# Kernel optimization log

Hardware: AMD Instinct MI355X
Metric: run time of the kernel (lower is better)

Reference implementation:

```python
import jax, jax.numpy as jnp
import numpy as np

NUM_HEADS = 4
OUTPUT_DIM = 32
NUM_NODES = 50000
NUM_EDGES = 800000
INPUT_DIM = 128


def setup_inputs() -> dict:
    key = jax.random.key(0)
    k1, k2, k3, k4 = jax.random.split(key, 4)
    node_features = jax.random.uniform(k1, (NUM_NODES, INPUT_DIM), dtype=jnp.float32)
    edge_index = jax.random.randint(k2, (2, NUM_EDGES), 0, NUM_NODES, dtype=jnp.int64)
    # Linear weight (xavier-like scale), stored as [in, out] for x @ W
    W = jax.random.normal(k3, (INPUT_DIM, NUM_HEADS * OUTPUT_DIM), dtype=jnp.float32) * 0.1
    att = jax.random.normal(k4, (2 * OUTPUT_DIM, 1), dtype=jnp.float32) * 0.2
    return {"node_features": node_features, "edge_index": edge_index, "W": W, "att": att}


def reference(node_features, edge_index, W, att):
    num_nodes = node_features.shape[0]
    # Linear projection -> [N, H, D]  (dropout = identity in eval mode)
    proj = (node_features @ W).reshape(num_nodes, NUM_HEADS, OUTPUT_DIM)
    src = proj[edge_index[0]]   # [E, H, D]
    tgt = proj[edge_index[1]]   # [E, H, D]
    # concat([src,tgt]) @ att  ==  src @ att[:D] + tgt @ att[D:]
    a_src = att[:OUTPUT_DIM, 0]   # [D]
    a_tgt = att[OUTPUT_DIM:, 0]   # [D]
    scores = jax.nn.leaky_relu(
        jnp.einsum('ehd,d->eh', src, a_src) + jnp.einsum('ehd,d->eh', tgt, a_tgt),
        negative_slope=0.01,
    )  # [E, H]
    # Faithful to original: softmax over the HEADS axis (dim=-1 of [E, H])
    alpha = jax.nn.softmax(scores, axis=-1)  # [E, H]
    weighted = tgt * alpha[..., None]        # [E, H, D]
    # index_add_ on dim 0 with edge_index[0]
    out = jax.ops.segment_sum(weighted, edge_index[0], num_segments=num_nodes)  # [N, H, D]
    # concat_heads=False -> mean over heads
    return out.mean(axis=1)  # [N, D]
```

## Files before the change

kernel.cpp:

```cpp
#include <hip/hip_runtime.h>
#include <math.h>

#define N_NODES 50000
#define N_EDGES 800000
#define IN_DIM 128
#define N_HEADS 4
#define OUT_DIM 32
#define PROJ_DIM 128
#define WSTR 144

#define NBIN 196
#define BINCAP 5000
#define MAXDEG 64

#define PROJ_BLKS 391
#define PART_BLKS 391
#define TOTAL_BLKS (PROJ_BLKS + PART_BLKS)

typedef short bf16x8 __attribute__((ext_vector_type(8)));
typedef float f32x4  __attribute__((ext_vector_type(4)));
typedef _Float16 h2  __attribute__((ext_vector_type(2)));

__device__ __forceinline__ ushort f32_to_bf16(float f) {
    unsigned u = __float_as_uint(f);
    unsigned r = u + 0x7fffu + ((u >> 16) & 1u);
    return (ushort)(r >> 16);
}

__device__ __forceinline__ float bf16_to_f32(ushort v) {
    return __uint_as_float((unsigned)v << 16);
}

__device__ __forceinline__ bf16x8 cvt8(float4 a, float4 b) {
    bf16x8 r;
    r[0] = (short)f32_to_bf16(a.x); r[1] = (short)f32_to_bf16(a.y);
    r[2] = (short)f32_to_bf16(a.z); r[3] = (short)f32_to_bf16(a.w);
    r[4] = (short)f32_to_bf16(b.x); r[5] = (short)f32_to_bf16(b.y);
    r[6] = (short)f32_to_bf16(b.z); r[7] = (short)f32_to_bf16(b.w);
    return r;
}

__global__ __launch_bounds__(256) void combo_kernel(
    const float* __restrict__ X, const float* __restrict__ W,
    const float* __restrict__ att, const int* __restrict__ ei,
    ushort* __restrict__ projT, float* __restrict__ s_src, float* __restrict__ s_tgt,
    int* __restrict__ bin_cursor, unsigned* __restrict__ slab)
{
    __shared__ ushort Wt[128 * WSTR];

    const int tid = threadIdx.x;

    if (blockIdx.x >= PROJ_BLKS) {
        int* cnt   = (int*)Wt;
        int* gbase = cnt + 256;

        for (int t = tid; t < NBIN; t += 256) cnt[t] = 0;
        __syncthreads();

        const int ebase = (blockIdx.x - PROJ_BLKS) * 2048;
        unsigned srcv[8], tgtv[8];
        int rank[8];
#pragma unroll
        for (int i = 0; i < 8; ++i) {
            int e = ebase + i * 256 + tid;
            bool ok = e < N_EDGES;
            srcv[i] = ok ? (unsigned)ei[e] : 0u;
            tgtv[i] = ok ? (unsigned)ei[N_EDGES + e] : 0u;
            rank[i] = ok ? atomicAdd(&cnt[srcv[i] >> 8], 1) : -1;
        }
        __syncthreads();

        for (int t = tid; t < NBIN; t += 256)
            gbase[t] = atomicAdd(&bin_cursor[t], cnt[t]);
        __syncthreads();

#pragma unroll
        for (int i = 0; i < 8; ++i) {
            if (rank[i] >= 0) {
                int bin = srcv[i] >> 8;
                int p = gbase[bin] + rank[i];
                if (p < BINCAP)
                    slab[bin * BINCAP + p] = (tgtv[i] << 16) | (srcv[i] & 255u);
            }
        }
        return;
    }

    for (int idx = tid; idx < 64 * 128; idx += 256) {
        int kp = idx >> 7;
        int c  = idx & 127;
        float w0 = W[(2 * kp) * PROJ_DIM + c];
        float w1 = W[(2 * kp + 1) * PROJ_DIM + c];
        unsigned pr = (unsigned)f32_to_bf16(w0) | ((unsigned)f32_to_bf16(w1) << 16);
        *(unsigned*)&Wt[c * WSTR + 2 * kp] = pr;
    }
    __syncthreads();

    const int wv   = tid >> 6;
    const int lane = tid & 63;
    const int m = lane & 15;
    const int q = lane >> 4;
    const int rbase = blockIdx.x * 128;

    int arow0 = rbase + wv * 32 + m;
    int arow1 = arow0 + 16;
    arow0 = (arow0 < N_NODES) ? arow0 : N_NODES - 1;
    arow1 = (arow1 < N_NODES) ? arow1 : N_NODES - 1;
    const long long xb0 = (long long)arow0 * IN_DIM;
    const long long xb1 = (long long)arow1 * IN_DIM;

    f32x4 acc[2][8];
#pragma unroll
    for (int rt = 0; rt < 2; ++rt)
#pragma unroll
        for (int ct = 0; ct < 8; ++ct) acc[rt][ct] = (f32x4){0.f, 0.f, 0.f, 0.f};

#pragma unroll
    for (int ks = 0; ks < 4; ++ks) {
        const int k0 = ks * 32 + q * 8;
        float4 a0lo = *(const float4*)&X[xb0 + k0];
        float4 a0hi = *(const float4*)&X[xb0 + k0 + 4];
        float4 a1lo = *(const float4*)&X[xb1 + k0];
        float4 a1hi = *(const float4*)&X[xb1 + k0 + 4];
        bf16x8 afrag0 = cvt8(a0lo, a0hi);
        bf16x8 afrag1 = cvt8(a1lo, a1hi);
#pragma unroll
        for (int ct = 0; ct < 8; ++ct) {
            bf16x8 bfrag = *(const bf16x8*)&Wt[(ct * 16 + m) * WSTR + k0];
            acc[0][ct] = __builtin_amdgcn_mfma_f32_16x16x32_bf16(afrag0, bfrag, acc[0][ct], 0, 0, 0);
            acc[1][ct] = __builtin_amdgcn_mfma_f32_16x16x32_bf16(afrag1, bfrag, acc[1][ct], 0, 0, 0);
        }
    }

    const float as_lo = att[m],      as_hi = att[m + 16];
    const float at_lo = att[32 + m], at_hi = att[48 + m];

#pragma unroll
    for (int rt = 0; rt < 2; ++rt) {
        const int rowb = rbase + wv * 32 + rt * 16 + q * 4;
#pragma unroll
        for (int r = 0; r < 4; ++r) {
            const int row = rowb + r;
            float cl[4], ch[4];
#pragma unroll
            for (int h = 0; h < 4; ++h) {
                cl[h] = acc[rt][2 * h][r];
                ch[h] = acc[rt][2 * h + 1][r];
            }
            if (row < N_NODES) {
                ushort4 plo, phi;
                plo.x = f32_to_bf16(cl[0]); plo.y = f32_to_bf16(cl[1]);
                plo.z = f32_to_bf16(cl[2]); plo.w = f32_to_bf16(cl[3]);
                phi.x = f32_to_bf16(ch[0]); phi.y = f32_to_bf16(ch[1]);
                phi.z = f32_to_bf16(ch[2]); phi.w = f32_to_bf16(ch[3]);
                *(ushort4*)&projT[(long long)row * PROJ_DIM + m * 4] = plo;
                *(ushort4*)&projT[(long long)row * PROJ_DIM + (m + 16) * 4] = phi;
            }
            float ps[4], pt[4];
#pragma unroll
            for (int h = 0; h < 4; ++h) {
                ps[h] = cl[h] * as_lo + ch[h] * as_hi;
                pt[h] = cl[h] * at_lo + ch[h] * at_hi;
            }
#pragma unroll
            for (int off = 8; off > 0; off >>= 1) {
#pragma unroll
                for (int h = 0; h < 4; ++h) {
                    ps[h] += __shfl_down(ps[h], off, 16);
                    pt[h] += __shfl_down(pt[h], off, 16);
                }
            }
            if (m == 0 && row < N_NODES) {
                *(float4*)&s_src[row * N_HEADS] = make_float4(ps[0], ps[1], ps[2], ps[3]);
                *(float4*)&s_tgt[row * N_HEADS] = make_float4(pt[0], pt[1], pt[2], pt[3]);
            }
        }
    }
}

__global__ __launch_bounds__(256) void binsort_kernel(
    const unsigned* __restrict__ slab, const int* __restrict__ bin_cursor,
    ushort* __restrict__ csr, int* __restrict__ offs, int* __restrict__ deg)
{
    __shared__ int cnt2[256];
    __shared__ int ex[256];
    __shared__ int wsum[4];
    __shared__ ushort stgt[BINCAP];

    const int b = blockIdx.x;
    const int t = threadIdx.x;
    const int lane = t & 63;
    const int wid  = t >> 6;
    int n_e = bin_cursor[b];
    n_e = (n_e < BINCAP) ? n_e : BINCAP;

    cnt2[t] = 0;
    __syncthreads();

    unsigned pk[20];
    int npk = 0;
    for (int i = t; i < n_e; i += 256) {
        unsigned v = slab[b * BINCAP + i];
        int node8 = v & 255u;
        int r = atomicAdd(&cnt2[node8], 1);
        r = (r < 255) ? r : 255;
        pk[npk++] = (v & 0xFFFF0000u) | ((unsigned)r << 8) | (unsigned)node8;
    }
    __syncthreads();

    const int v = cnt2[t];
    int x = v;
#pragma unroll
    for (int off = 1; off < 64; off <<= 1) {
        int y = __shfl_up(x, off);
        x += (lane >= off) ? y : 0;
    }
    if (lane == 63) wsum[wid] = x;
    __syncthreads();
    int add = 0;
#pragma unroll
    for (int w = 0; w < 4; ++w) add += (w < wid) ? wsum[w] : 0;
    ex[t] = x + add - v;
    __syncthreads();

    for (int j = 0; j < npk; ++j) {
        unsigned pv = pk[j];
        int lpos = ex[pv & 255u] + (int)((pv >> 8) & 255u);
        if (lpos < BINCAP) stgt[lpos] = (ushort)(pv >> 16);
    }
    __syncthreads();

    for (int i = t; i < n_e; i += 256) csr[b * BINCAP + i] = stgt[i];
    int node = b * 256 + t;
    if (node < N_NODES) {
        offs[node] = b * BINCAP + ex[t];
        deg[node]  = cnt2[t];
    }
}

__global__ __launch_bounds__(256) void gather_kernel(
    const int* __restrict__ deg, const int* __restrict__ offs,
    const ushort* __restrict__ csr,
    const float* __restrict__ s_src, const float* __restrict__ s_tgt,
    const ushort* __restrict__ projT, float* __restrict__ out)
{
    const int wv   = threadIdx.x >> 6;
    const int lane = threadIdx.x & 63;
    const int node = blockIdx.x * 4 + wv;

    int n = deg[node];
    n = (n < MAXDEG) ? n : MAXDEG;
    const int o = offs[node];

    int mytgt = 0, myA01 = 0, myA23 = 0;
    if (lane < n) {
        int tgt = csr[o + lane];
        float4 ss = *(const float4*)&s_src[node * N_HEADS];
        float4 st = *(const float4*)&s_tgt[tgt * N_HEADS];

        float sc[4] = { ss.x + st.x, ss.y + st.y, ss.z + st.z, ss.w + st.w };
        float mx = -1e30f;
#pragma unroll
        for (int h = 0; h < 4; ++h) {
            sc[h] = (sc[h] > 0.0f) ? sc[h] : 0.01f * sc[h];
            mx = fmaxf(mx, sc[h]);
        }
        float sum = 0.0f;
#pragma unroll
        for (int h = 0; h < 4; ++h) {
            sc[h] = __expf(sc[h] - mx);
            sum += sc[h];
        }
        float inv = 0.25f / sum;

        h2 a01, a23;
        a01.x = (_Float16)(sc[0] * inv);
        a01.y = (_Float16)(sc[1] * inv);
        a23.x = (_Float16)(sc[2] * inv);
        a23.y = (_Float16)(sc[3] * inv);
        mytgt = tgt;
        myA01 = __builtin_bit_cast(int, a01);
        myA23 = __builtin_bit_cast(int, a23);
    }

    const int d    = lane & 31;
    const int half = lane >> 5;

    float acc0 = 0.0f, acc1 = 0.0f, acc2 = 0.0f, acc3 = 0.0f;

    for (int j = 0; j < n; j += 16) {
        int tg[8], ea[8], eb[8];
#pragma unroll
        for (int u = 0; u < 8; ++u) {
            int sl = j + 2 * u + half;
            bool ok = sl < n;
            int slc = ok ? sl : 0;
            int tgv = __shfl(mytgt, slc);
            int eav = __shfl(myA01, slc);
            int ebv = __shfl(myA23, slc);
            tg[u] = tgv;
            ea[u] = ok ? eav : 0;
            eb[u] = ok ? ebv : 0;
        }
        ushort4 p[8];
#pragma unroll
        for (int u = 0; u < 8; ++u)
            p[u] = *(const ushort4*)&projT[(long long)tg[u] * PROJ_DIM + d * 4];
#pragma unroll
        for (int u = 0; u < 8; ++u) {
            h2 a = __builtin_bit_cast(h2, ea[u]);
            h2 b = __builtin_bit_cast(h2, eb[u]);
            float* accp = (u & 1) ? ((u & 2) ? &acc3 : &acc1)
                                  : ((u & 2) ? &acc2 : &acc0);
            float tt = *accp;
            tt = fmaf((float)a.x, bf16_to_f32(p[u].x), tt);
            tt = fmaf((float)a.y, bf16_to_f32(p[u].y), tt);
            tt = fmaf((float)b.x, bf16_to_f32(p[u].z), tt);
            tt = fmaf((float)b.y, bf16_to_f32(p[u].w), tt);
            *accp = tt;
        }
    }

    float acc = (acc0 + acc1) + (acc2 + acc3);
    acc += __shfl_down(acc, 32);
    if (lane < 32) out[node * OUT_DIM + d] = acc;
}

extern "C" void kernel_launch(void* const* d_in, const int* in_sizes, int n_in,
                              void* d_out, int out_size, void* d_ws, size_t ws_size,
                              hipStream_t stream) {
    const float* X   = (const float*)d_in[0];
    const int*   ei  = (const int*)d_in[1];
    const float* W   = (const float*)d_in[2];
    const float* att = (const float*)d_in[3];
    float* out = (float*)d_out;

    char* p = (char*)d_ws;
    ushort* projT   = (ushort*)p;   p += (size_t)N_NODES * PROJ_DIM * 2;
    float* s_src    = (float*)p;    p += (size_t)N_NODES * N_HEADS * 4;
    float* s_tgt    = (float*)p;    p += (size_t)N_NODES * N_HEADS * 4;
    unsigned* slab  = (unsigned*)p; p += (size_t)NBIN * BINCAP * 4;
    ushort* csr     = (ushort*)p;   p += (size_t)NBIN * BINCAP * 2;
    int* offs       = (int*)p;      p += (size_t)N_NODES * 4;
    int* deg        = (int*)p;      p += (size_t)N_NODES * 4;
    int* bin_cursor = (int*)p;      p += 256 * 4;

    (void)hipMemsetAsync(bin_cursor, 0, 256 * sizeof(int), stream);

    combo_kernel<<<TOTAL_BLKS, 256, 0, stream>>>(
        X, W, att, ei, projT, s_src, s_tgt, bin_cursor, slab);

    binsort_kernel<<<NBIN, 256, 0, stream>>>(slab, bin_cursor, csr, offs, deg);

    gather_kernel<<<N_NODES / 4, 256, 0, stream>>>(
        deg, offs, csr, s_src, s_tgt, projT, out);
}
```

Baseline: 145.2 us.

## Replace two-pass bin sort with direct per-node fixed-slot adjacency via global atomics

Drops the shared-memory binning pass and the separate binsort kernel. Each edge now claims a slot in a fixed 64-entry per-node adjacency array through a global atomicAdd on the node's degree counter. The gather kernel indexes that array by node*MAXDEG instead of a computed offset. This saves one kernel launch and the slab round trip, but adds about 800k global atomics with scattered 2-byte writes and a larger memset of the degree array.

```diff
diff --git a/kernel.cpp b/kernel.cpp
--- a/kernel.cpp
+++ b/kernel.cpp
@@ -9,8 +9,6 @@
 #define PROJ_DIM 128
 #define WSTR 144
 
-#define NBIN 196
-#define BINCAP 5000
 #define MAXDEG 64
 
 #define PROJ_BLKS 391
@@ -44,43 +42,23 @@
     const float* __restrict__ X, const float* __restrict__ W,
     const float* __restrict__ att, const int* __restrict__ ei,
     ushort* __restrict__ projT, float* __restrict__ s_src, float* __restrict__ s_tgt,
-    int* __restrict__ bin_cursor, unsigned* __restrict__ slab)
+    int* __restrict__ deg, ushort* __restrict__ csr)
 {
     __shared__ ushort Wt[128 * WSTR];
 
     const int tid = threadIdx.x;
 
     if (blockIdx.x >= PROJ_BLKS) {
-        int* cnt   = (int*)Wt;
-        int* gbase = cnt + 256;
-
-        for (int t = tid; t < NBIN; t += 256) cnt[t] = 0;
-        __syncthreads();
-
         const int ebase = (blockIdx.x - PROJ_BLKS) * 2048;
-        unsigned srcv[8], tgtv[8];
-        int rank[8];
 #pragma unroll
         for (int i = 0; i < 8; ++i) {
             int e = ebase + i * 256 + tid;
-            bool ok = e < N_EDGES;
-            srcv[i] = ok ? (unsigned)ei[e] : 0u;
-            tgtv[i] = ok ? (unsigned)ei[N_EDGES + e] : 0u;
-            rank[i] = ok ? atomicAdd(&cnt[srcv[i] >> 8], 1) : -1;
-        }
-        __syncthreads();
-
-        for (int t = tid; t < NBIN; t += 256)
-            gbase[t] = atomicAdd(&bin_cursor[t], cnt[t]);
-        __syncthreads();
-
-#pragma unroll
-        for (int i = 0; i < 8; ++i) {
-            if (rank[i] >= 0) {
-                int bin = srcv[i] >> 8;
-                int p = gbase[bin] + rank[i];
-                if (p < BINCAP)
-                    slab[bin * BINCAP + p] = (tgtv[i] << 16) | (srcv[i] & 255u);
+            if (e < N_EDGES) {
+                unsigned s = (unsigned)ei[e];
+                unsigned t = (unsigned)ei[N_EDGES + e];
+                int r = atomicAdd(&deg[s], 1);
+                if (r < MAXDEG)
+                    csr[(long long)s * MAXDEG + r] = (ushort)t;
             }
         }
         return;
@@ -178,69 +156,8 @@
     }
 }
 
-__global__ __launch_bounds__(256) void binsort_kernel(
-    const unsigned* __restrict__ slab, const int* __restrict__ bin_cursor,
-    ushort* __restrict__ csr, int* __restrict__ offs, int* __restrict__ deg)
-{
-    __shared__ int cnt2[256];
-    __shared__ int ex[256];
-    __shared__ int wsum[4];
-    __shared__ ushort stgt[BINCAP];
-
-    const int b = blockIdx.x;
-    const int t = threadIdx.x;
-    const int lane = t & 63;
-    const int wid  = t >> 6;
-    int n_e = bin_cursor[b];
-    n_e = (n_e < BINCAP) ? n_e : BINCAP;
-
-    cnt2[t] = 0;
-    __syncthreads();
-
-    unsigned pk[20];
-    int npk = 0;
-    for (int i = t; i < n_e; i += 256) {
-        unsigned v = slab[b * BINCAP + i];
-        int node8 = v & 255u;
-        int r = atomicAdd(&cnt2[node8], 1);
-        r = (r < 255) ? r : 255;
-        pk[npk++] = (v & 0xFFFF0000u) | ((unsigned)r << 8) | (unsigned)node8;
-    }
-    __syncthreads();
-
-    const int v = cnt2[t];
-    int x = v;
-#pragma unroll
-    for (int off = 1; off < 64; off <<= 1) {
-        int y = __shfl_up(x, off);
-        x += (lane >= off) ? y : 0;
-    }
-    if (lane == 63) wsum[wid] = x;
-    __syncthreads();
-    int add = 0;
-#pragma unroll
-    for (int w = 0; w < 4; ++w) add += (w < wid) ? wsum[w] : 0;
-    ex[t] = x + add - v;
-    __syncthreads();
-
-    for (int j = 0; j < npk; ++j) {
-        unsigned pv = pk[j];
-        int lpos = ex[pv & 255u] + (int)((pv >> 8) & 255u);
-        if (lpos < BINCAP) stgt[lpos] = (ushort)(pv >> 16);
-    }
-    __syncthreads();
-
-    for (int i = t; i < n_e; i += 256) csr[b * BINCAP + i] = stgt[i];
-    int node = b * 256 + t;
-    if (node < N_NODES) {
-        offs[node] = b * BINCAP + ex[t];
-        deg[node]  = cnt2[t];
-    }
-}
-
 __global__ __launch_bounds__(256) void gather_kernel(
-    const int* __restrict__ deg, const int* __restrict__ offs,
-    const ushort* __restrict__ csr,
+    const int* __restrict__ deg, const ushort* __restrict__ csr,
     const float* __restrict__ s_src, const float* __restrict__ s_tgt,
     const ushort* __restrict__ projT, float* __restrict__ out)
 {
@@ -250,7 +167,7 @@
 
     int n = deg[node];
     n = (n < MAXDEG) ? n : MAXDEG;
-    const int o = offs[node];
+    const long long o = (long long)node * MAXDEG;
 
     int mytgt = 0, myA01 = 0, myA23 = 0;
     if (lane < n) {
@@ -339,19 +256,14 @@
     ushort* projT   = (ushort*)p;   p += (size_t)N_NODES * PROJ_DIM * 2;
     float* s_src    = (float*)p;    p += (size_t)N_NODES * N_HEADS * 4;
     float* s_tgt    = (float*)p;    p += (size_t)N_NODES * N_HEADS * 4;
-    unsigned* slab  = (unsigned*)p; p += (size_t)NBIN * BINCAP * 4;
-    ushort* csr     = (ushort*)p;   p += (size_t)NBIN * BINCAP * 2;
-    int* offs       = (int*)p;      p += (size_t)N_NODES * 4;
+    ushort* csr     = (ushort*)p;   p += (size_t)N_NODES * MAXDEG * 2;
     int* deg        = (int*)p;      p += (size_t)N_NODES * 4;
-    int* bin_cursor = (int*)p;      p += 256 * 4;
-
-    (void)hipMemsetAsync(bin_cursor, 0, 256 * sizeof(int), stream);
+
+    (void)hipMemsetAsync(deg, 0, (size_t)N_NODES * sizeof(int), stream);
 
     combo_kernel<<<TOTAL_BLKS, 256, 0, stream>>>(
-        X, W, att, ei, projT, s_src, s_tgt, bin_cursor, slab);
-
-    binsort_kernel<<<NBIN, 256, 0, stream>>>(slab, bin_cursor, csr, offs, deg);
+        X, W, att, ei, projT, s_src, s_tgt, deg, csr);
 
     gather_kernel<<<N_NODES / 4, 256, 0, stream>>>(
-        deg, offs, csr, s_src, s_tgt, projT, out);
-}
+        deg, csr, s_src, s_tgt, projT, out);
+}
```

Result: slower. 151.2 us (+4.1%).

## Regroup stages: run partition alone, fuse bin sort with projection GEMM

Applied to the files above, without the earlier changes.

Edge partitioning moves into its own small kernel. The per-bin counting sort is merged into the projection GEMM kernel as extra blocks, so the sort overlaps with the matmul instead of running as a separate serialized launch after it. Shared memory is reused from the weight tile buffer for the sort scratch. The kernel count stays the same, but the lightweight partition kernel now runs alone, and the fused kernel's blocks have uneven work.

```diff
diff --git a/kernel.cpp b/kernel.cpp
--- a/kernel.cpp
+++ b/kernel.cpp
@@ -15,7 +15,7 @@
 
 #define PROJ_BLKS 391
 #define PART_BLKS 391
-#define TOTAL_BLKS (PROJ_BLKS + PART_BLKS)
+#define FUSE_BLKS (NBIN + PROJ_BLKS)
 
 typedef short bf16x8 __attribute__((ext_vector_type(8)));
 typedef float f32x4  __attribute__((ext_vector_type(4)));
@@ -40,48 +40,113 @@
     return r;
 }
 
-__global__ __launch_bounds__(256) void combo_kernel(
+__global__ __launch_bounds__(256) void partition_kernel(
+    const int* __restrict__ ei, int* __restrict__ bin_cursor,
+    unsigned* __restrict__ slab)
+{
+    __shared__ int cnt[256];
+    __shared__ int gbase[256];
+
+    const int tid = threadIdx.x;
+
+    for (int t = tid; t < NBIN; t += 256) cnt[t] = 0;
+    __syncthreads();
+
+    const int ebase = blockIdx.x * 2048;
+    unsigned srcv[8], tgtv[8];
+    int rank[8];
+#pragma unroll
+    for (int i = 0; i < 8; ++i) {
+        int e = ebase + i * 256 + tid;
+        bool ok = e < N_EDGES;
+        srcv[i] = ok ? (unsigned)ei[e] : 0u;
+        tgtv[i] = ok ? (unsigned)ei[N_EDGES + e] : 0u;
+        rank[i] = ok ? atomicAdd(&cnt[srcv[i] >> 8], 1) : -1;
+    }
+    __syncthreads();
+
+    for (int t = tid; t < NBIN; t += 256)
+        gbase[t] = atomicAdd(&bin_cursor[t], cnt[t]);
+    __syncthreads();
+
+#pragma unroll
+    for (int i = 0; i < 8; ++i) {
+        if (rank[i] >= 0) {
+            int bin = srcv[i] >> 8;
+            int p = gbase[bin] + rank[i];
+            if (p < BINCAP)
+                slab[bin * BINCAP + p] = (tgtv[i] << 16) | (srcv[i] & 255u);
+        }
+    }
+}
+
+__global__ __launch_bounds__(256) void fused_kernel(
     const float* __restrict__ X, const float* __restrict__ W,
-    const float* __restrict__ att, const int* __restrict__ ei,
+    const float* __restrict__ att,
+    const unsigned* __restrict__ slab, const int* __restrict__ bin_cursor,
     ushort* __restrict__ projT, float* __restrict__ s_src, float* __restrict__ s_tgt,
-    int* __restrict__ bin_cursor, unsigned* __restrict__ slab)
+    ushort* __restrict__ csr, int* __restrict__ offs, int* __restrict__ deg)
 {
     __shared__ ushort Wt[128 * WSTR];
 
     const int tid = threadIdx.x;
 
-    if (blockIdx.x >= PROJ_BLKS) {
-        int* cnt   = (int*)Wt;
-        int* gbase = cnt + 256;
-
-        for (int t = tid; t < NBIN; t += 256) cnt[t] = 0;
-        __syncthreads();
-
-        const int ebase = (blockIdx.x - PROJ_BLKS) * 2048;
-        unsigned srcv[8], tgtv[8];
-        int rank[8];
-#pragma unroll
-        for (int i = 0; i < 8; ++i) {
-            int e = ebase + i * 256 + tid;
-            bool ok = e < N_EDGES;
-            srcv[i] = ok ? (unsigned)ei[e] : 0u;
-            tgtv[i] = ok ? (unsigned)ei[N_EDGES + e] : 0u;
-            rank[i] = ok ? atomicAdd(&cnt[srcv[i] >> 8], 1) : -1;
-        }
-        __syncthreads();
-
-        for (int t = tid; t < NBIN; t += 256)
-            gbase[t] = atomicAdd(&bin_cursor[t], cnt[t]);
-        __syncthreads();
-
-#pragma unroll
-        for (int i = 0; i < 8; ++i) {
-            if (rank[i] >= 0) {
-                int bin = srcv[i] >> 8;
-                int p = gbase[bin] + rank[i];
-                if (p < BINCAP)
-                    slab[bin * BINCAP + p] = (tgtv[i] << 16) | (srcv[i] & 255u);
-            }
+    if (blockIdx.x < NBIN) {
+        int*    cnt2 = (int*)Wt;
+        int*    ex   = cnt2 + 256;
+        int*    wsum = ex + 256;
+        ushort* stgt = (ushort*)(wsum + 8);
+
+        const int b = blockIdx.x;
+        const int t = tid;
+        const int lane = t & 63;
+        const int wid  = t >> 6;
+        int n_e = bin_cursor[b];
+        n_e = (n_e < BINCAP) ? n_e : BINCAP;
+
+        cnt2[t] = 0;
+        __syncthreads();
+
+        unsigned pk[20];
+        int npk = 0;
+        for (int i = t; i < n_e; i += 256) {
+            unsigned v = slab[b * BINCAP + i];
+            int node8 = v & 255u;
+            int r = atomicAdd(&cnt2[node8], 1);
+            r = (r < 255) ? r : 255;
+            pk[npk++] = (v & 0xFFFF0000u) | ((unsigned)r << 8) | (unsigned)node8;
+        }
+        __syncthreads();
+
+        const int v = cnt2[t];
+        int x = v;
+#pragma unroll
+        for (int off = 1; off < 64; off <<= 1) {
+            int y = __shfl_up(x, off);
+            x += (lane >= off) ? y : 0;
+        }
+        if (lane == 63) wsum[wid] = x;
+        __syncthreads();
+        int add = 0;
+#pragma unroll
+        for (int w = 0; w < 4; ++w) add += (w < wid) ? wsum[w] : 0;
+        const int myex = x + add - v;
+        const int mycnt = v;
+        ex[t] = myex;
+        __syncthreads();
+
+        for (int j = 0; j < npk; ++j) {
+            unsigned pv = pk[j];
+            int lpos = ex[pv & 255u] + (int)((pv >> 8) & 255u);
+            if (lpos < BINCAP) stgt[lpos] = (ushort)(pv >> 16);
+        }
+        __syncthreads();
+
+        for (int i = t; i < n_e; i += 256) csr[b * BINCAP + i] = stgt[i];
+        int node = b * 256 + t;
+        if (node < N_NODES) {
+            offs[node] = b * BINCAP + myex;
+            deg[node]  = mycnt;
         }
         return;
     }
@@ -100,7 +165,7 @@
     const int lane = tid & 63;
     const int m = lane & 15;
     const int q = lane >> 4;
-    const int rbase = blockIdx.x * 128;
+    const int rbase = (blockIdx.x - NBIN) * 128;
 
     int arow0 = rbase + wv * 32 + m;
     int arow1 = arow0 + 16;
@@ -175,66 +240,6 @@
                 *(float4*)&s_tgt[row * N_HEADS] = make_float4(pt[0], pt[1], pt[2], pt[3]);
             }
         }
-    }
-}
-
-__global__ __launch_bounds__(256) void binsort_kernel(
-    const unsigned* __restrict__ slab, const int* __restrict__ bin_cursor,
-    ushort* __restrict__ csr, int* __restrict__ offs, int* __restrict__ deg)
-{
-    __shared__ int cnt2[256];
-    __shared__ int ex[256];
-    __shared__ int wsum[4];
-    __shared__ ushort stgt[BINCAP];
-
-    const int b = blockIdx.x;
-    const int t = threadIdx.x;
-    const int lane = t & 63;
-    const int wid  = t >> 6;
-    int n_e = bin_cursor[b];
-    n_e = (n_e < BINCAP) ? n_e : BINCAP;
-
-    cnt2[t] = 0;
-    __syncthreads();
-
-    unsigned pk[20];
-    int npk = 0;
-    for (int i = t; i < n_e; i += 256) {
-        unsigned v = slab[b * BINCAP + i];
-        int node8 = v & 255u;
-        int r = atomicAdd(&cnt2[node8], 1);
-        r = (r < 255) ? r : 255;
-        pk[npk++] = (v & 0xFFFF0000u) | ((unsigned)r << 8) | (unsigned)node8;
-    }
-    __syncthreads();
-
-    const int v = cnt2[t];
-    int x = v;
-#pragma unroll
-    for (int off = 1; off < 64; off <<= 1) {
-        int y = __shfl_up(x, off);
-        x += (lane >= off) ? y : 0;
-    }
-    if (lane == 63) wsum[wid] = x;
-    __syncthreads();
-    int add = 0;
-#pragma unroll
-    for (int w = 0; w < 4; ++w) add += (w < wid) ? wsum[w] : 0;
-    ex[t] = x + add - v;
-    __syncthreads();
-
-    for (int j = 0; j < npk; ++j) {
-        unsigned pv = pk[j];
-        int lpos = ex[pv & 255u] + (int)((pv >> 8) & 255u);
-        if (lpos < BINCAP) stgt[lpos] = (ushort)(pv >> 16);
-    }
-    __syncthreads();
-
-    for (int i = t; i < n_e; i += 256) csr[b * BINCAP + i] = stgt[i];
-    int node = b * 256 + t;
-    if (node < N_NODES) {
-        offs[node] = b * BINCAP + ex[t];
-        deg[node]  = cnt2[t];
     }
 }
 
@@ -347,10 +352,10 @@
 
     (void)hipMemsetAsync(bin_cursor, 0, 256 * sizeof(int), stream);
 
-    combo_kernel<<<TOTAL_BLKS, 256, 0, stream>>>(
-        X, W, att, ei, projT, s_src, s_tgt, bin_cursor, slab);
-
-    binsort_kernel<<<NBIN, 256, 0, stream>>>(slab, bin_cursor, csr, offs, deg);
+    partition_kernel<<<PART_BLKS, 256, 0, stream>>>(ei, bin_cursor, slab);
+
+    fused_kernel<<<FUSE_BLKS, 256, 0, stream>>>(
+        X, W, att, slab, bin_cursor, projT, s_src, s_tgt, csr, offs, deg);
 
     gather_kernel<<<N_NODES / 4, 256, 0, stream>>>(
         deg, offs, csr, s_src, s_tgt, projT, out);
```

After: 142.1 us. -2.2%, faster.
